# Kernel optimization log

Hardware: AMD Instinct MI355X
Metric: run time of the kernel (lower is better)

Reference implementation:

```python
import jax, jax.numpy as jnp
import numpy as np


def setup_inputs() -> dict:
    key = jax.random.key(0)
    B, U, I, H = 8192, 16, 128, 128
    k = jax.random.split(key, 6)
    s = 1.0 / np.sqrt(H)  # PyTorch GRU init scale (uniform(-s, s)); use scaled normal for test data
    return {
        "inputs": jax.random.normal(k[0], (B, U, I), dtype=jnp.float32),
        "hidden": jax.random.normal(k[1], (B, U, H), dtype=jnp.float32),
        "w_ih": jax.random.normal(k[2], (U, 3 * H, I), dtype=jnp.float32) * s,
        "w_hh": jax.random.normal(k[3], (U, 3 * H, H), dtype=jnp.float32) * s,
        "b_ih": jax.random.normal(k[4], (U, 3 * H), dtype=jnp.float32) * s,
        "b_hh": jax.random.normal(k[5], (U, 3 * H), dtype=jnp.float32) * s,
    }


def reference(inputs, hidden, w_ih, w_hh, b_ih, b_hh):
    # Grouped single-step GRU: one independent GRU cell per unit u, batched via einsum.
    # PyTorch GRU gate order in the 3H dim: [reset, update, new].
    H = hidden.shape[-1]
    # gates_x[b,u,g] = sum_i inputs[b,u,i] * w_ih[u,g,i] + b_ih[u,g]
    gx = jnp.einsum("bui,ugi->bug", inputs, w_ih) + b_ih  # (B, U, 3H)
    gh = jnp.einsum("buh,ugh->bug", hidden, w_hh) + b_hh  # (B, U, 3H)
    xr, xz, xn = gx[..., :H], gx[..., H:2 * H], gx[..., 2 * H:]
    hr, hz, hn = gh[..., :H], gh[..., H:2 * H], gh[..., 2 * H:]
    r = jax.nn.sigmoid(xr + hr)
    z = jax.nn.sigmoid(xz + hz)
    n = jnp.tanh(xn + r * hn)
    return (1.0 - z) * n + z * hidden  # (B, U, H)
```

## Files before the change

### kernel.cpp

```cpp
#include <hip/hip_runtime.h>
#include <hip/hip_bf16.h>

typedef __attribute__((ext_vector_type(8))) short  short8;
typedef __attribute__((ext_vector_type(4))) float  floatx4;

#define UH   2048
#define XPAD 264

#define MFMA16(a,b,c) __builtin_amdgcn_mfma_f32_16x16x32_bf16(a, b, c, 0, 0, 0)

static __device__ __forceinline__ unsigned int pkbf16(float a, float b) {
    __hip_bfloat162 p = __float22bfloat162_rn(make_float2(a, b));
    return *(unsigned int*)&p;
}
static __device__ __forceinline__ float bf2f(unsigned short h) {
    unsigned int u = (unsigned int)h << 16;
    return *(float*)&u;
}

__global__ __launch_bounds__(512, 2) void gru_fused(
    const float* __restrict__ inputs, const float* __restrict__ hidden,
    const float* __restrict__ w_ih,   const float* __restrict__ w_hh,
    const float* __restrict__ b_ih,   const float* __restrict__ b_hh,
    float* __restrict__ out)
{
    __shared__ __align__(16) __hip_bfloat16 Xs[2][64][XPAD];

    const int bx   = blockIdx.x;
    const int u    = ((bx & 7) << 1) | ((bx >> 3) & 1);
    const int mt0  = (bx >> 4) * 8;
    const int tid  = threadIdx.x;
    const int lane = tid & 63;
    const int wv   = tid >> 6;
    const int lr   = lane & 15;
    const int lq   = lane >> 4;

    auto loadW = [&](int gt, int s) -> short8 {
        const int row = gt * 16 + lr;
        const int k0  = s * 32 + lq * 8;
        const float* src = (k0 < 128)
            ? (w_ih + (size_t)(u * 384 + row) * 128 + k0)
            : (w_hh + (size_t)(u * 384 + row) * 128 + (k0 - 128));
        float4 v0 = ((const float4*)src)[0];
        float4 v1 = ((const float4*)src)[1];
        union { uint4 q; short8 s8; } cvt;
        cvt.q.x = pkbf16(v0.x, v0.y);
        cvt.q.y = pkbf16(v0.z, v0.w);
        cvt.q.z = pkbf16(v1.x, v1.y);
        cvt.q.w = pkbf16(v1.z, v1.w);
        return cvt.s8;
    };
    short8 fR[8], fZ[8], fN[8];
    #pragma unroll
    for (int s = 0; s < 8; ++s) {
        fR[s] = loadW(     wv, s);
        fZ[s] = loadW( 8 + wv, s);
        fN[s] = loadW(16 + wv, s);
    }

    const int c0 = wv * 16 + lq * 4;
    float4 bi = *(const float4*)(b_ih + u * 384 +       c0);
    float4 bh = *(const float4*)(b_hh + u * 384 +       c0);
    float4 zi = *(const float4*)(b_ih + u * 384 + 128 + c0);
    float4 zh = *(const float4*)(b_hh + u * 384 + 128 + c0);
    float4 ni = *(const float4*)(b_ih + u * 384 + 256 + c0);
    float4 nh = *(const float4*)(b_hh + u * 384 + 256 + c0);
    const floatx4 accR0  = (floatx4){bi.x + bh.x, bi.y + bh.y, bi.z + bh.z, bi.w + bh.w};
    const floatx4 accZ0  = (floatx4){zi.x + zh.x, zi.y + zh.y, zi.z + zh.z, zi.w + zh.w};
    const floatx4 accXN0 = (floatx4){ni.x, ni.y, ni.z, ni.w};
    const floatx4 accHN0 = (floatx4){nh.x, nh.y, nh.z, nh.w};

    const int scol = (tid & 63) * 4;
    const float* sbase = ((scol < 128) ? (inputs + scol)
                                       : (hidden + (scol - 128)))
                       + (size_t)u * 128;

    float4 stg[8];

    auto ISSUE = [&](int mt) {
        const float* p = sbase + (size_t)(mt * 64 + wv) * UH;
        #pragma unroll
        for (int i = 0; i < 8; ++i)
            stg[i] = *(const float4*)(p + (size_t)(i * 8) * UH);
    };
    auto WRITE = [&](int buf) {
        #pragma unroll
        for (int i = 0; i < 8; ++i) {
            uint2 w;
            w.x = pkbf16(stg[i].x, stg[i].y);
            w.y = pkbf16(stg[i].z, stg[i].w);
            *(uint2*)&Xs[buf][i * 8 + wv][scol] = w;
        }
    };
    auto BARRIER = [&]() {
        asm volatile("s_waitcnt lgkmcnt(0)" ::: "memory");
        __builtin_amdgcn_sched_barrier(0);
        __builtin_amdgcn_s_barrier();
        __builtin_amdgcn_sched_barrier(0);
    };

    ISSUE(mt0 + 0);
    #pragma unroll
    for (int s = 0; s < 8; ++s) {
        asm volatile("" : "+v"(fR[s]));
        asm volatile("" : "+v"(fZ[s]));
        asm volatile("" : "+v"(fN[s]));
    }
    WRITE(0);
    ISSUE(mt0 + 1);
    BARRIER();

    #pragma unroll 1
    for (int j = 0; j < 8; ++j) {
        const int buf = j & 1;

        floatx4 aR[4], aZ[4], aXN[4], aHN[4];
        #pragma unroll
        for (int m4 = 0; m4 < 4; ++m4) {
            aR[m4]  = accR0;
            aZ[m4]  = accZ0;
            aXN[m4] = accXN0;
            aHN[m4] = accHN0;
        }
        #pragma unroll
        for (int s = 0; s < 8; ++s) {
            short8 xF[4];
            #pragma unroll
            for (int m4 = 0; m4 < 4; ++m4)
                xF[m4] = *(const short8*)((const short*)&Xs[buf][m4 * 16 + lr][0]
                                          + s * 32 + lq * 8);
            #pragma unroll
            for (int m4 = 0; m4 < 4; ++m4) {
                aR[m4] = MFMA16(fR[s], xF[m4], aR[m4]);
                aZ[m4] = MFMA16(fZ[s], xF[m4], aZ[m4]);
                if (s < 4) aXN[m4] = MFMA16(fN[s], xF[m4], aXN[m4]);
                else       aHN[m4] = MFMA16(fN[s], xF[m4], aHN[m4]);
            }
        }

        if (j < 7) {
            WRITE(buf ^ 1);
            if (j < 6) ISSUE(mt0 + j + 2);
        }

        #pragma unroll
        for (int m4 = 0; m4 < 4; ++m4) {
            const int m = m4 * 16 + lr;
            ushort4 hq = *(const ushort4*)&Xs[buf][m][128 + c0];
            unsigned short hs[4] = {hq.x, hq.y, hq.z, hq.w};
            float4 o;
            float* op = (float*)&o;
            #pragma unroll
            for (int r = 0; r < 4; ++r) {
                float rv = __builtin_amdgcn_rcpf(1.f + __expf(-aR[m4][r]));
                float zv = __builtin_amdgcn_rcpf(1.f + __expf(-aZ[m4][r]));
                float npre = aXN[m4][r] + rv * aHN[m4][r];
                float nv = 2.f * __builtin_amdgcn_rcpf(1.f + __expf(-2.f * npre)) - 1.f;
                float hv = bf2f(hs[r]);
                op[r] = nv + zv * (hv - nv);
            }
            float* orow = out + (size_t)((mt0 + j) * 64 + m) * UH + u * 128 + c0;
            *(float4*)orow = o;
        }

        if (j < 7) BARRIER();
    }
}


extern "C" void kernel_launch(void* const* d_in, const int* in_sizes, int n_in,
                              void* d_out, int out_size, void* d_ws, size_t ws_size,
                              hipStream_t stream) {
    const float* inputs = (const float*)d_in[0];
    const float* hidden = (const float*)d_in[1];
    const float* w_ih   = (const float*)d_in[2];
    const float* w_hh   = (const float*)d_in[3];
    const float* b_ih   = (const float*)d_in[4];
    const float* b_hh   = (const float*)d_in[5];
    float* out = (float*)d_out;

    gru_fused<<<dim3(256), dim3(512), 0, stream>>>(inputs, hidden,
                                                   w_ih, w_hh, b_ih, b_hh, out);
}
```

Before: 202.8 us.

## Swizzle LDS tile, swap MFMA operands, double grid with 4 tiles per block

Replaces the padded LDS row layout with an XOR swizzle, so reads and writes avoid bank conflicts without padding. Swaps the MFMA operand order so each lane holds an output column and per-lane scalar biases are added in the epilogue instead of seeding the accumulators. Doubles the grid to 512 blocks, each processing 4 row tiles instead of 8, and raises the launch-bounds occupancy hint to 4. Output stores become scalar strided writes instead of float4, which may cost store efficiency, and the higher occupancy target may force register spills given the large per-thread weight fragments.

```diff
diff --git a/kernel.cpp b/kernel.cpp
--- a/kernel.cpp
+++ b/kernel.cpp
@@ -5,7 +5,7 @@
 typedef __attribute__((ext_vector_type(4))) float  floatx4;
 
 #define UH   2048
-#define XPAD 264
+#define XPAD 256
 
 #define MFMA16(a,b,c) __builtin_amdgcn_mfma_f32_16x16x32_bf16(a, b, c, 0, 0, 0)
 
@@ -13,12 +13,8 @@
     __hip_bfloat162 p = __float22bfloat162_rn(make_float2(a, b));
     return *(unsigned int*)&p;
 }
-static __device__ __forceinline__ float bf2f(unsigned short h) {
-    unsigned int u = (unsigned int)h << 16;
-    return *(float*)&u;
-}
 
-__global__ __launch_bounds__(512, 2) void gru_fused(
+__global__ __launch_bounds__(512, 4) void gru_fused(
     const float* __restrict__ inputs, const float* __restrict__ hidden,
     const float* __restrict__ w_ih,   const float* __restrict__ w_hh,
     const float* __restrict__ b_ih,   const float* __restrict__ b_hh,
@@ -28,7 +24,7 @@
 
     const int bx   = blockIdx.x;
     const int u    = ((bx & 7) << 1) | ((bx >> 3) & 1);
-    const int mt0  = (bx >> 4) * 8;
+    const int mt0  = (bx >> 4) * 4;
     const int tid  = threadIdx.x;
     const int lane = tid & 63;
     const int wv   = tid >> 6;
@@ -58,17 +54,11 @@
         fN[s] = loadW(16 + wv, s);
     }
 
-    const int c0 = wv * 16 + lq * 4;
-    float4 bi = *(const float4*)(b_ih + u * 384 +       c0);
-    float4 bh = *(const float4*)(b_hh + u * 384 +       c0);
-    float4 zi = *(const float4*)(b_ih + u * 384 + 128 + c0);
-    float4 zh = *(const float4*)(b_hh + u * 384 + 128 + c0);
-    float4 ni = *(const float4*)(b_ih + u * 384 + 256 + c0);
-    float4 nh = *(const float4*)(b_hh + u * 384 + 256 + c0);
-    const floatx4 accR0  = (floatx4){bi.x + bh.x, bi.y + bh.y, bi.z + bh.z, bi.w + bh.w};
-    const floatx4 accZ0  = (floatx4){zi.x + zh.x, zi.y + zh.y, zi.z + zh.z, zi.w + zh.w};
-    const floatx4 accXN0 = (floatx4){ni.x, ni.y, ni.z, ni.w};
-    const floatx4 accHN0 = (floatx4){nh.x, nh.y, nh.z, nh.w};
+    const int   c   = wv * 16 + lr;
+    const float br  = b_ih[u * 384 +       c] + b_hh[u * 384 +       c];
+    const float bz  = b_ih[u * 384 + 128 + c] + b_hh[u * 384 + 128 + c];
+    const float bxn = b_ih[u * 384 + 256 + c];
+    const float bhn = b_hh[u * 384 + 256 + c];
 
     const int scol = (tid & 63) * 4;
     const float* sbase = ((scol < 128) ? (inputs + scol)
@@ -89,7 +79,8 @@
             uint2 w;
             w.x = pkbf16(stg[i].x, stg[i].y);
             w.y = pkbf16(stg[i].z, stg[i].w);
-            *(uint2*)&Xs[buf][i * 8 + wv][scol] = w;
+            char* rowp = (char*)&Xs[buf][i * 8 + wv][0];
+            *(uint2*)(rowp + ((lane * 8) ^ (wv << 4))) = w;
         }
     };
     auto BARRIER = [&]() {
@@ -100,70 +91,62 @@
     };
 
     ISSUE(mt0 + 0);
-    #pragma unroll
-    for (int s = 0; s < 8; ++s) {
-        asm volatile("" : "+v"(fR[s]));
-        asm volatile("" : "+v"(fZ[s]));
-        asm volatile("" : "+v"(fN[s]));
-    }
     WRITE(0);
     ISSUE(mt0 + 1);
     BARRIER();
 
     #pragma unroll 1
-    for (int j = 0; j < 8; ++j) {
+    for (int j = 0; j < 4; ++j) {
         const int buf = j & 1;
 
         floatx4 aR[4], aZ[4], aXN[4], aHN[4];
         #pragma unroll
         for (int m4 = 0; m4 < 4; ++m4) {
-            aR[m4]  = accR0;
-            aZ[m4]  = accZ0;
-            aXN[m4] = accXN0;
-            aHN[m4] = accHN0;
+            aR[m4]  = (floatx4){0.f, 0.f, 0.f, 0.f};
+            aZ[m4]  = (floatx4){0.f, 0.f, 0.f, 0.f};
+            aXN[m4] = (floatx4){0.f, 0.f, 0.f, 0.f};
+            aHN[m4] = (floatx4){0.f, 0.f, 0.f, 0.f};
         }
         #pragma unroll
         for (int s = 0; s < 8; ++s) {
             short8 xF[4];
             #pragma unroll
-            for (int m4 = 0; m4 < 4; ++m4)
-                xF[m4] = *(const short8*)((const short*)&Xs[buf][m4 * 16 + lr][0]
-                                          + s * 32 + lq * 8);
+            for (int m4 = 0; m4 < 4; ++m4) {
+                const char* rowp = (const char*)&Xs[buf][m4 * 16 + lr][0];
+                xF[m4] = *(const short8*)(rowp
+                           + ((s * 64 + lq * 16) ^ ((lr & 7) << 4)));
+            }
             #pragma unroll
             for (int m4 = 0; m4 < 4; ++m4) {
-                aR[m4] = MFMA16(fR[s], xF[m4], aR[m4]);
-                aZ[m4] = MFMA16(fZ[s], xF[m4], aZ[m4]);
-                if (s < 4) aXN[m4] = MFMA16(fN[s], xF[m4], aXN[m4]);
-                else       aHN[m4] = MFMA16(fN[s], xF[m4], aHN[m4]);
+                aR[m4] = MFMA16(xF[m4], fR[s], aR[m4]);
+                aZ[m4] = MFMA16(xF[m4], fZ[s], aZ[m4]);
+                if (s < 4) aXN[m4] = MFMA16(xF[m4], fN[s], aXN[m4]);
+                else       aHN[m4] = MFMA16(xF[m4], fN[s], aHN[m4]);
             }
         }
 
-        if (j < 7) {
-            WRITE(buf ^ 1);
-            if (j < 6) ISSUE(mt0 + j + 2);
+        float* obase = out + (size_t)(mt0 + j) * 64 * UH + u * 128 + c;
+        #pragma unroll
+        for (int m4 = 0; m4 < 4; ++m4) {
+            #pragma unroll
+            for (int r = 0; r < 4; ++r) {
+                const int m = m4 * 16 + lq * 4 + r;
+                float rv = __builtin_amdgcn_rcpf(1.f + __expf(-(aR[m4][r] + br)));
+                float zv = __builtin_amdgcn_rcpf(1.f + __expf(-(aZ[m4][r] + bz)));
+                float npre = (aXN[m4][r] + bxn) + rv * (aHN[m4][r] + bhn);
+                float nv = 2.f * __builtin_amdgcn_rcpf(1.f + __expf(-2.f * npre)) - 1.f;
+                const char* rowp = (const char*)&Xs[buf][m][0];
+                float hv = __bfloat162float(*(const __hip_bfloat16*)(rowp
+                             + ((256 + 2 * c) ^ ((m & 7) << 4))));
+                obase[(size_t)m * UH] = nv + zv * (hv - nv);
+            }
         }
 
-        #pragma unroll
-        for (int m4 = 0; m4 < 4; ++m4) {
-            const int m = m4 * 16 + lr;
-            ushort4 hq = *(const ushort4*)&Xs[buf][m][128 + c0];
-            unsigned short hs[4] = {hq.x, hq.y, hq.z, hq.w};
-            float4 o;
-            float* op = (float*)&o;
-            #pragma unroll
-            for (int r = 0; r < 4; ++r) {
-                float rv = __builtin_amdgcn_rcpf(1.f + __expf(-aR[m4][r]));
-                float zv = __builtin_amdgcn_rcpf(1.f + __expf(-aZ[m4][r]));
-                float npre = aXN[m4][r] + rv * aHN[m4][r];
-                float nv = 2.f * __builtin_amdgcn_rcpf(1.f + __expf(-2.f * npre)) - 1.f;
-                float hv = bf2f(hs[r]);
-                op[r] = nv + zv * (hv - nv);
-            }
-            float* orow = out + (size_t)((mt0 + j) * 64 + m) * UH + u * 128 + c0;
-            *(float4*)orow = o;
+        if (j < 3) {
+            WRITE(buf ^ 1);
+            if (j < 2) ISSUE(mt0 + j + 2);
+            BARRIER();
         }
-
-        if (j < 7) BARRIER();
     }
 }
 
@@ -179,6 +162,6 @@
     const float* b_hh   = (const float*)d_in[5];
     float* out = (float*)d_out;
 
-    gru_fused<<<dim3(256), dim3(512), 0, stream>>>(inputs, hidden,
+    gru_fused<<<dim3(512), dim3(512), 0, stream>>>(inputs, hidden,
                                                    w_ih, w_hh, b_ih, b_hh, out);
 }
```

Result: slower. 299.2 us (+47.5%).
